# Kernel tuning notes

Hardware: AMD Instinct MI355X
Metric: run time of the kernel (lower is better)

Reference implementation:

```python
import jax, jax.numpy as jnp
import numpy as np

CLASSES = (32, 32)
SUPERCLASSES = 8
OVERALL = CLASSES[0] * CLASSES[1]
CLASS_FACTOR = OVERALL // SUPERCLASSES


def lrelu(x):
    return jax.nn.leaky_relu(x, 0.01)


def conv1x1(x, w, b):
    # x: [B,C,H,W], w: [O,C], b: [O]
    return jnp.einsum('oc,bchw->bohw', w, x) + b[None, :, None, None]


def cond_mul(x, inds, W, b):
    # x: [N,I], inds: [N] int, W: [K,I,O], b: [K,O]
    return jnp.einsum('ni,nio->no', x, W[inds]) + b[inds]


def setup_inputs() -> dict:
    key = jax.random.key(0)
    ks = jax.random.split(key, 24)
    s = 0.05
    d = {}
    d['x_in'] = jax.random.normal(ks[0], (1, 128, 192, 256), dtype=jnp.float32)
    # mask branch
    d['Wm1'] = jax.random.normal(ks[1], (32, 128)) * s
    d['bm1'] = jnp.zeros((32,), jnp.float32)
    d['Wm2'] = jax.random.normal(ks[2], (16, 32)) * s
    d['bm2'] = jnp.zeros((16,), jnp.float32)
    d['Wm3'] = jax.random.normal(ks[3], (1, 16)) * s
    d['bm3'] = jnp.zeros((1,), jnp.float32)
    # classification branch
    d['Wcl1'] = jax.random.normal(ks[4], (128, 128)) * s
    d['bcl1'] = jnp.zeros((128,), jnp.float32)
    d['Wcl21'] = jax.random.normal(ks[5], (128, 128)) * s
    d['bcl21'] = jnp.zeros((128,), jnp.float32)
    d['Wcl31'] = jax.random.normal(ks[6], (32, 128)) * s
    d['bcl31'] = jnp.zeros((32,), jnp.float32)
    d['Wcl22'] = jax.random.normal(ks[7], (CLASSES[0], 128, 32)) * s  # CondMul
    d['bcl22'] = jnp.zeros((CLASSES[0], 32), jnp.float32)
    d['Wcl32'] = jax.random.normal(ks[8], (CLASSES[0], 32, CLASSES[1])) * s
    d['bcl32'] = jnp.zeros((CLASSES[0], CLASSES[1]), jnp.float32)
    d['Wr1'] = jax.random.normal(ks[9], (128, 128)) * s
    d['br1'] = jnp.zeros((128,), jnp.float32)
    d['Wr2'] = jax.random.normal(ks[10], (SUPERCLASSES, 128, 32)) * s
    d['br2'] = jnp.zeros((SUPERCLASSES, 32), jnp.float32)
    d['Wr3'] = jax.random.normal(ks[11], (OVERALL, 32, 1)) * s
    d['br3'] = jnp.zeros((OVERALL, 1), jnp.float32)
    return d


def reference(x_in, Wm1, bm1, Wm2, bm2, Wm3, bm3,
              Wcl1, bcl1, Wcl21, bcl21, Wcl31, bcl31,
              Wcl22, bcl22, Wcl32, bcl32,
              Wr1, br1, Wr2, br2, Wr3, br3):
    B = x_in.shape[0]
    # mask branch
    m = lrelu(conv1x1(x_in, Wm1, bm1))
    m = lrelu(conv1x1(m, Wm2, bm2))
    mask = lrelu(conv1x1(m, Wm3, bm3))
    # classification branch
    x = lrelu(conv1x1(x_in, Wcl1, bcl1))          # [B,128,H,W]
    # torch: transpose(1,3) -> [B,W,H,C], flatten
    x_l = jnp.transpose(x, (0, 3, 2, 1)).reshape(-1, x.shape[1])
    x2 = lrelu(conv1x1(x, Wcl21, bcl21))
    cl1 = conv1x1(x2, Wcl31, bcl31)               # [B,classes0,H,W]
    inds1 = jnp.argmax(cl1, axis=1).reshape(-1).astype(jnp.int32)  # [N] (B,H,W order)
    h = lrelu(cond_mul(x_l, inds1, Wcl22, bcl22))  # [N,32]
    h = cond_mul(h, inds1, Wcl32, bcl32)           # [N,classes1]
    inds2 = jnp.argmax(h, axis=1).astype(jnp.int32)
    inds = inds1 * CLASSES[1] + inds2
    inds_r = jnp.clip(inds, 0, OVERALL - 1).astype(jnp.int32)
    inds_super = jnp.clip(inds_r // CLASS_FACTOR, 0, SUPERCLASSES - 1)
    r = lrelu(conv1x1(x_in, Wr1, br1))
    r_l = jnp.transpose(r, (0, 3, 2, 1)).reshape(-1, r.shape[1])
    r2 = lrelu(cond_mul(r_l, inds_super, Wr2, br2))  # [N,32]
    regression = cond_mul(r2, inds_r, Wr3, br3)      # [N,1]
    regression = regression.reshape(B, 1, 1, -1)
    inds = inds.reshape(regression.shape)
    x_real = (inds.astype(jnp.float32) + regression) * (1.0 / float(OVERALL))
    return (x_real, mask)
```

## Files before the change

kernel.cpp:

```cpp
#include <hip/hip_runtime.h>

#define HH 192
#define WW 256
#define NPIX (HH*WW)
#define NSEG (NPIX/64)

__device__ __forceinline__ float lrelu(float v) { return v > 0.0f ? v : 0.01f * v; }

__device__ __forceinline__ unsigned short bfhi(float x) {
    unsigned b = __float_as_uint(x);
    return (unsigned short)((b + 0x7FFFu + ((b >> 16) & 1u)) >> 16);
}
__device__ __forceinline__ float bff(unsigned short u) {
    return __uint_as_float(((unsigned)u) << 16);
}

typedef __attribute__((ext_vector_type(8))) short short8v;
typedef __attribute__((ext_vector_type(4))) short short4v;
typedef __attribute__((ext_vector_type(4))) float f32x4;

__global__ __launch_bounds__(256, 3) void k_fused1(
    const float* __restrict__ X,
    const float* __restrict__ Wcl1, const float* __restrict__ bcl1,
    const float* __restrict__ Wr1,  const float* __restrict__ br1,
    const float* __restrict__ Wm1,  const float* __restrict__ bm1,
    const float* __restrict__ Wm2,  const float* __restrict__ bm2,
    const float* __restrict__ Wm3,  const float* __restrict__ bm3,
    float* __restrict__ x_t, float* __restrict__ r_t,
    float* __restrict__ out)
{
    __shared__ float smem[10240];

    const int tid = threadIdx.x;
    const int q0  = blockIdx.x * 128;

    if (blockIdx.y == 2) {
        unsigned short* Wmhi = (unsigned short*)smem;
        unsigned short* Wmlo = Wmhi + 1280;
        unsigned short* Xthi = Wmlo + 1280;
        unsigned short* Xtlo = Xthi + 5120;
        float (*m1b)[33] = (float(*)[33])smem;

        const int l = tid & 63;
        const int w = tid >> 6;
        const int c = l & 15;
        const int g = l >> 4;

        float bvm[2][4];
        #pragma unroll
        for (int ot = 0; ot < 2; ++ot)
            #pragma unroll
            for (int r = 0; r < 4; ++r)
                bvm[ot][r] = bm1[ot * 16 + g * 4 + r];

        f32x4 accM[2][2];
        #pragma unroll
        for (int ot = 0; ot < 2; ++ot)
            #pragma unroll
            for (int pi = 0; pi < 2; ++pi) {
                accM[ot][pi][0] = bvm[ot][0]; accM[ot][pi][1] = bvm[ot][1];
                accM[ot][pi][2] = bvm[ot][2]; accM[ot][pi][3] = bvm[ot][3];
            }

        const int sx_px = tid & 127;
        const int sx_kh = (tid >> 7) * 16;
        const float* Xp = X + q0 + sx_px;

        for (int k0 = 0; k0 < 128; k0 += 32) {
            {
                float xv[16];
                #pragma unroll
                for (int i = 0; i < 16; ++i)
                    xv[i] = Xp[(size_t)(k0 + sx_kh + i) * NPIX];
                #pragma unroll
                for (int j = 0; j < 2; ++j) {
                    short8v hv, lv;
                    #pragma unroll
                    for (int i = 0; i < 8; ++i) {
                        unsigned short h = bfhi(xv[j * 8 + i]);
                        hv[i] = (short)h;
                        lv[i] = (short)bfhi(xv[j * 8 + i] - bff(h));
                    }
                    int gg = (sx_kh >> 3) + j;
                    int gs = gg ^ ((sx_px >> 3) & 3);
                    *(short8v*)(Xthi + sx_px * 40 + gs * 8) = hv;
                    *(short8v*)(Xtlo + sx_px * 40 + gs * 8) = lv;
                }
            }
            {
                int o = tid >> 3, kc = (tid & 7) * 4;
                float4 v = *(const float4*)(Wm1 + o * 128 + k0 + kc);
                float wv[4] = {v.x, v.y, v.z, v.w};
                short4v hv, lv;
                #pragma unroll
                for (int i = 0; i < 4; ++i) {
                    unsigned short h = bfhi(wv[i]);
                    hv[i] = (short)h;
                    lv[i] = (short)bfhi(wv[i] - bff(h));
                }
                int gg = kc >> 3;
                int gs = gg ^ (o & 3);
                int addr = o * 40 + gs * 8 + (kc & 7);
                *(short4v*)(Wmhi + addr) = hv;
                *(short4v*)(Wmlo + addr) = lv;
            }
            __syncthreads();

            short8v ahi[2], alo[2];
            #pragma unroll
            for (int ot = 0; ot < 2; ++ot) {
                int row = ot * 16 + c;
                int ao = row * 40 + (g ^ (row & 3)) * 8;
                ahi[ot] = *(const short8v*)(Wmhi + ao);
                alo[ot] = *(const short8v*)(Wmlo + ao);
            }
            #pragma unroll
            for (int pi = 0; pi < 2; ++pi) {
                int row = (2 * w + pi) * 16 + c;
                int bo = row * 40 + (g ^ ((row >> 3) & 3)) * 8;
                short8v bhi = *(const short8v*)(Xthi + bo);
                short8v blo = *(const short8v*)(Xtlo + bo);
                #pragma unroll
                for (int ot = 0; ot < 2; ++ot) {
                    accM[ot][pi] = __builtin_amdgcn_mfma_f32_16x16x32_bf16(
                        ahi[ot], bhi, accM[ot][pi], 0, 0, 0);
                    accM[ot][pi] = __builtin_amdgcn_mfma_f32_16x16x32_bf16(
                        ahi[ot], blo, accM[ot][pi], 0, 0, 0);
                    accM[ot][pi] = __builtin_amdgcn_mfma_f32_16x16x32_bf16(
                        alo[ot], bhi, accM[ot][pi], 0, 0, 0);
                }
            }
            __syncthreads();
        }
        #pragma unroll
        for (int pi = 0; pi < 2; ++pi) {
            int px = (2 * w + pi) * 16 + c;
            #pragma unroll
            for (int ot = 0; ot < 2; ++ot)
                #pragma unroll
                for (int r = 0; r < 4; ++r)
                    m1b[px][ot * 16 + g * 4 + r] = lrelu(accM[ot][pi][r]);
        }
        __syncthreads();
        if (tid < 128) {
            float m3 = bm3[0];
            #pragma unroll 2
            for (int j = 0; j < 16; ++j) {
                float s = bm2[j];
                #pragma unroll
                for (int k = 0; k < 32; ++k)
                    s = fmaf(Wm2[j * 32 + k], m1b[tid][k], s);
                m3 = fmaf(Wm3[j], lrelu(s), m3);
            }
            out[NPIX + q0 + tid] = lrelu(m3);
        }
        return;
    }

    {
        const bool exact = (blockIdx.y == 0);
        const float* __restrict__ Wsrc = exact ? Wcl1 : Wr1;
        const float* __restrict__ bsrc = exact ? bcl1 : br1;
        float* __restrict__ osrc       = exact ? x_t : r_t;

        unsigned short* Whi  = (unsigned short*)smem;
        unsigned short* Wlo  = Whi  + 5120;
        unsigned short* Xthi = Wlo  + 5120;
        unsigned short* Xtlo = Xthi + 5120;

        const int l = tid & 63;
        const int w = tid >> 6;
        const int c = l & 15;
        const int g = l >> 4;
        const int o0 = w * 32;

        float bv[2][4];
        #pragma unroll
        for (int ot = 0; ot < 2; ++ot)
            #pragma unroll
            for (int r = 0; r < 4; ++r)
                bv[ot][r] = bsrc[o0 + ot * 16 + g * 4 + r];

        f32x4 acc[2][8];
        #pragma unroll
        for (int ot = 0; ot < 2; ++ot)
            #pragma unroll
            for (int pt = 0; pt < 8; ++pt) {
                acc[ot][pt][0] = bv[ot][0]; acc[ot][pt][1] = bv[ot][1];
                acc[ot][pt][2] = bv[ot][2]; acc[ot][pt][3] = bv[ot][3];
            }

        const int sx_px = tid & 127;
        const int sx_kh = (tid >> 7) * 16;
        const float* Xp = X + q0 + sx_px;

        for (int k0 = 0; k0 < 128; k0 += 32) {
            {
                float xv[16];
                #pragma unroll
                for (int i = 0; i < 16; ++i)
                    xv[i] = Xp[(size_t)(k0 + sx_kh + i) * NPIX];
                #pragma unroll
                for (int j = 0; j < 2; ++j) {
                    short8v hv, lv;
                    #pragma unroll
                    for (int i = 0; i < 8; ++i) {
                        unsigned short h = bfhi(xv[j * 8 + i]);
                        hv[i] = (short)h;
                        lv[i] = (short)bfhi(xv[j * 8 + i] - bff(h));
                    }
                    int gg = (sx_kh >> 3) + j;
                    int gs = gg ^ ((sx_px >> 3) & 3);
                    *(short8v*)(Xthi + sx_px * 40 + gs * 8) = hv;
                    *(short8v*)(Xtlo + sx_px * 40 + gs * 8) = lv;
                }
            }
            #pragma unroll
            for (int p = 0; p < 4; ++p) {
                int lin = p * 1024 + tid * 4;
                int o = lin >> 5, kc = lin & 31;
                float4 v = *(const float4*)(Wsrc + o * 128 + k0 + kc);
                float wv[4] = {v.x, v.y, v.z, v.w};
                short4v hv, lv;
                #pragma unroll
                for (int i = 0; i < 4; ++i) {
                    unsigned short h = bfhi(wv[i]);
                    hv[i] = (short)h;
                    lv[i] = (short)bfhi(wv[i] - bff(h));
                }
                int gg = kc >> 3;
                int gs = gg ^ (o & 3);
                int addr = o * 40 + gs * 8 + (kc & 7);
                *(short4v*)(Whi + addr) = hv;
                *(short4v*)(Wlo + addr) = lv;
            }
            __syncthreads();

            short8v ahi[2], alo[2];
            #pragma unroll
            for (int ot = 0; ot < 2; ++ot) {
                int row = o0 + ot * 16 + c;
                int ao = row * 40 + (g ^ (row & 3)) * 8;
                ahi[ot] = *(const short8v*)(Whi + ao);
                alo[ot] = *(const short8v*)(Wlo + ao);
            }
            #pragma unroll
            for (int pt = 0; pt < 8; ++pt) {
                int row = pt * 16 + c;
                int bo = row * 40 + (g ^ ((row >> 3) & 3)) * 8;
                short8v bhi = *(const short8v*)(Xthi + bo);
                short8v blo = *(const short8v*)(Xtlo + bo);
                #pragma unroll
                for (int ot = 0; ot < 2; ++ot) {
                    acc[ot][pt] = __builtin_amdgcn_mfma_f32_16x16x32_bf16(
                        ahi[ot], bhi, acc[ot][pt], 0, 0, 0);
                    acc[ot][pt] = __builtin_amdgcn_mfma_f32_16x16x32_bf16(
                        ahi[ot], blo, acc[ot][pt], 0, 0, 0);
                    acc[ot][pt] = __builtin_amdgcn_mfma_f32_16x16x32_bf16(
                        alo[ot], bhi, acc[ot][pt], 0, 0, 0);
                    if (exact)
                        acc[ot][pt] = __builtin_amdgcn_mfma_f32_16x16x32_bf16(
                            alo[ot], blo, acc[ot][pt], 0, 0, 0);
                }
            }
            __syncthreads();
        }

        #pragma unroll
        for (int pt = 0; pt < 8; ++pt) {
            int px = pt * 16 + c;
            int q  = q0 + px;
            int np = (q & 255) * 192 + (q >> 8);
            float* op = osrc + (size_t)np * 128;
            #pragma unroll
            for (int ot = 0; ot < 2; ++ot) {
                float4 o4;
                o4.x = lrelu(acc[ot][pt][0]); o4.y = lrelu(acc[ot][pt][1]);
                o4.z = lrelu(acc[ot][pt][2]); o4.w = lrelu(acc[ot][pt][3]);
                *(float4*)(op + o0 + ot * 16 + g * 4) = o4;
            }
        }
    }
}

__global__ __launch_bounds__(256, 3) void k1b(
    const float* __restrict__ x_t,
    const float* __restrict__ Wcl21, const float* __restrict__ bcl21,
    const float* __restrict__ Wcl31, const float* __restrict__ bcl31,
    int* __restrict__ inds1_q)
{
    __shared__ float smem[8576];
    float (*As)[132]    = (float(*)[132])smem;
    float (*Ws)[132]    = (float(*)[132])(smem + 2112);
    float (*W31)[132]   = (float(*)[132])smem;
    float (*x2t)[68]    = (float(*)[68])(smem + 4224);
    float (*cl1buf)[33] = (float(*)[33])(smem + 4224);

    const int tid = threadIdx.x;
    const int n0  = blockIdx.x * 64;
    const int tcA = tid & 15, trA = tid >> 4;

    float acc[4][8];
    #pragma unroll
    for (int i = 0; i < 4; ++i)
        #pragma unroll
        for (int j = 0; j < 8; ++j)
            acc[i][j] = bcl21[(j >> 2) * 64 + trA * 4 + (j & 3)];

    for (int k0 = 0; k0 < 128; k0 += 16) {
        {
            int lin = tid * 4;
            int px = lin >> 4, kc = lin & 15;
            float4 v = *(const float4*)(x_t + (size_t)(n0 + px) * 128 + k0 + kc);
            As[kc + 0][px] = v.x; As[kc + 1][px] = v.y;
            As[kc + 2][px] = v.z; As[kc + 3][px] = v.w;
        }
        #pragma unroll
        for (int p = 0; p < 2; ++p) {
            int lin = p * 256 + tid;
            int r = lin >> 2, kc = (lin & 3) * 4;
            float4 v = *(const float4*)(Wcl21 + r * 128 + k0 + kc);
            Ws[kc + 0][r] = v.x; Ws[kc + 1][r] = v.y;
            Ws[kc + 2][r] = v.z; Ws[kc + 3][r] = v.w;
        }
        __syncthreads();
        #pragma unroll
        for (int kk = 0; kk < 16; ++kk) {
            float4 a  = *(const float4*)(&As[kk][tcA * 4]);
            float4 w0 = *(const float4*)(&Ws[kk][trA * 4]);
            float4 w1 = *(const float4*)(&Ws[kk][64 + trA * 4]);
            float av[4] = {a.x,a.y,a.z,a.w};
            float wv[8] = {w0.x,w0.y,w0.z,w0.w,w1.x,w1.y,w1.z,w1.w};
            #pragma unroll
            for (int i = 0; i < 4; ++i)
                #pragma unroll
                for (int j = 0; j < 8; ++j)
                    acc[i][j] = fmaf(av[i], wv[j], acc[i][j]);
        }
        __syncthreads();
    }

    const int tcB = tid & 15;
    const int trB = tid >> 4;
    float accB[4][2];
    #pragma unroll
    for (int i = 0; i < 4; ++i)
        #pragma unroll
        for (int j = 0; j < 2; ++j)
            accB[i][j] = bcl31[trB * 2 + j];

    #pragma unroll
    for (int p = 0; p < 4; ++p) {
        int lin = p * 1024 + tid * 4;
        int row = lin >> 7, kc = lin & 127;
        *(float4*)(&W31[row][kc]) = *(const float4*)(Wcl31 + row * 128 + kc);
    }
    #pragma unroll
    for (int j = 0; j < 4; ++j) {
        float4 o;
        o.x = lrelu(acc[0][j]); o.y = lrelu(acc[1][j]);
        o.z = lrelu(acc[2][j]); o.w = lrelu(acc[3][j]);
        *(float4*)(&x2t[trA * 4 + j][tcA * 4]) = o;
    }
    __syncthreads();
    for (int k = 0; k < 64; ++k) {
        float4 a = *(const float4*)(&x2t[k][tcB * 4]);
        float av[4] = {a.x,a.y,a.z,a.w};
        float w0 = W31[trB * 2 + 0][k];
        float w1 = W31[trB * 2 + 1][k];
        #pragma unroll
        for (int i = 0; i < 4; ++i) {
            accB[i][0] = fmaf(av[i], w0, accB[i][0]);
            accB[i][1] = fmaf(av[i], w1, accB[i][1]);
        }
    }
    __syncthreads();
    #pragma unroll
    for (int j = 0; j < 4; ++j) {
        float4 o;
        o.x = lrelu(acc[0][4+j]); o.y = lrelu(acc[1][4+j]);
        o.z = lrelu(acc[2][4+j]); o.w = lrelu(acc[3][4+j]);
        *(float4*)(&x2t[trA * 4 + j][tcA * 4]) = o;
    }
    __syncthreads();
    for (int k = 0; k < 64; ++k) {
        float4 a = *(const float4*)(&x2t[k][tcB * 4]);
        float av[4] = {a.x,a.y,a.z,a.w};
        float w0 = W31[trB * 2 + 0][64 + k];
        float w1 = W31[trB * 2 + 1][64 + k];
        #pragma unroll
        for (int i = 0; i < 4; ++i) {
            accB[i][0] = fmaf(av[i], w0, accB[i][0]);
            accB[i][1] = fmaf(av[i], w1, accB[i][1]);
        }
    }
    __syncthreads();

    #pragma unroll
    for (int i = 0; i < 4; ++i)
        #pragma unroll
        for (int j = 0; j < 2; ++j)
            cl1buf[tcB * 4 + i][trB * 2 + j] = accB[i][j];
    __syncthreads();
    if (tid < 64) {
        float bv = cl1buf[tid][0]; int bi = 0;
        #pragma unroll
        for (int c = 1; c < 32; ++c) {
            float v = cl1buf[tid][c];
            if (v > bv) { bv = v; bi = c; }
        }
        int n = n0 + tid;
        int w = n / 192, hh = n - w * 192;
        inds1_q[hh * 256 + w] = bi;
    }
}

__global__ void k_hist(const int* __restrict__ inds1_q, int* __restrict__ bh) {
    int tid = threadIdx.x;
    int n = blockIdx.x * 256 + tid;
    int key = inds1_q[n];
    int lane = tid & 63;
    int cnt = 0;
    for (int k = 0; k < 32; ++k) {
        unsigned long long m = __ballot(key == k);
        if (lane == k) cnt = __popcll(m);
    }
    if (lane < 32) bh[(n >> 6) * 32 + lane] = cnt;
}

__global__ void k_scanA(const int* __restrict__ bh, int* __restrict__ ebb,
                        int* __restrict__ total) {
    __shared__ int s[256];
    const int k = blockIdx.x, t = threadIdx.x;
    int v0 = bh[(t * 3 + 0) * 32 + k];
    int v1 = bh[(t * 3 + 1) * 32 + k];
    int v2 = bh[(t * 3 + 2) * 32 + k];
    int sum = v0 + v1 + v2;
    s[t] = sum; __syncthreads();
    for (int d = 1; d < 256; d <<= 1) {
        int x = (t >= d) ? s[t - d] : 0;
        __syncthreads();
        s[t] += x;
        __syncthreads();
    }
    int ex = s[t] - sum;
    ebb[(t * 3 + 0) * 32 + k] = ex;
    ebb[(t * 3 + 1) * 32 + k] = ex + v0;
    ebb[(t * 3 + 2) * 32 + k] = ex + v0 + v1;
    if (t == 255) total[k] = s[255];
}

__global__ void k_scatter2(const int* __restrict__ inds1_q,
                           const int* __restrict__ ebb,
                           const int* __restrict__ total,
                           int* __restrict__ order)
{
    __shared__ int ttot[32];
    const int tid = threadIdx.x;
    if (tid < 32) ttot[tid] = total[tid];
    __syncthreads();
    int n = blockIdx.x * 256 + tid;
    int key = inds1_q[n];
    int lane = tid & 63;
    unsigned long long peers = 0;
    for (int k = 0; k < 32; ++k) {
        unsigned long long m = __ballot(key == k);
        if (key == k) peers = m;
    }
    int rank = __popcll(peers & ((1ull << lane) - 1ull));
    int cbase = 0;
    #pragma unroll
    for (int k = 0; k < 32; ++k) cbase += (k < key) ? ttot[k] : 0;
    order[cbase + ebb[(n >> 6) * 32 + key] + rank] = n;
}

__global__ __launch_bounds__(256, 4) void k2h(
    const float* __restrict__ x_t,
    const float* __restrict__ Wcl22, const float* __restrict__ bcl22,
    const float* __restrict__ Wcl32, const float* __restrict__ bcl32,
    const int* __restrict__ total, const int* __restrict__ order,
    int* __restrict__ ind_ord)
{
    __shared__ float Was[4096];
    __shared__ float Wbs[1024];
    __shared__ int cpre[33];
    __shared__ int cbase[33];
    __shared__ int ttot[32];

    const int tid = threadIdx.x;
    if (tid < 32) ttot[tid] = total[tid];
    __syncthreads();
    if (tid == 0) {
        int s = 0, cb = 0;
        for (int k = 0; k < 32; ++k) {
            cpre[k] = s; cbase[k] = cb;
            int c = ttot[k];
            s += (c + 255) >> 8;
            cb += c;
        }
        cpre[32] = s; cbase[32] = cb;
    }
    __syncthreads();
    const int ci = blockIdx.x;
    if (ci >= cpre[32]) return;
    int cls = 0;
    while (cpre[cls + 1] <= ci) ++cls;
    const int st   = (ci - cpre[cls]) * 256;
    const int npx  = min(256, ttot[cls] - st);
    const int base = cbase[cls] + st;

    {
        const float4* ws = (const float4*)(Wcl22 + cls * 4096);
        #pragma unroll
        for (int j = 0; j < 4; ++j) ((float4*)Was)[j * 256 + tid] = ws[j * 256 + tid];
        ((float4*)Wbs)[tid] = ((const float4*)(Wcl32 + cls * 1024))[tid];
    }
    __syncthreads();

    const int m = order[base + min(tid, npx - 1)];
    const float4* xp = (const float4*)(x_t + (size_t)m * 128);

    float h[32];
    #pragma unroll
    for (int j = 0; j < 32; ++j) h[j] = bcl22[cls * 32 + j];
    #pragma unroll 2
    for (int c4 = 0; c4 < 32; ++c4) {
        float4 xv = xp[c4];
        float xa[4] = {xv.x, xv.y, xv.z, xv.w};
        #pragma unroll
        for (int cc = 0; cc < 4; ++cc) {
            const float* wr = &Was[(c4 * 4 + cc) * 32];
            #pragma unroll
            for (int j = 0; j < 32; ++j) h[j] = fmaf(xa[cc], wr[j], h[j]);
        }
    }
    #pragma unroll
    for (int j = 0; j < 32; ++j) h[j] = lrelu(h[j]);

    float g[32];
    #pragma unroll
    for (int j = 0; j < 32; ++j) g[j] = bcl32[cls * 32 + j];
    #pragma unroll 2
    for (int c = 0; c < 32; ++c) {
        float hv = h[c];
        const float* wr = &Wbs[c * 32];
        #pragma unroll
        for (int j = 0; j < 32; ++j) g[j] = fmaf(hv, wr[j], g[j]);
    }
    float bv = g[0]; int bi = 0;
    #pragma unroll
    for (int j = 1; j < 32; ++j)
        if (g[j] > bv) { bv = g[j]; bi = j; }
    if (tid < npx) ind_ord[base + tid] = cls * 32 + bi;
}

__global__ __launch_bounds__(256, 4) void k2r(
    const float* __restrict__ r_t,
    const float* __restrict__ Wr2,  const float* __restrict__ br2,
    const float* __restrict__ Wr3,  const float* __restrict__ br3,
    const int* __restrict__ total, const int* __restrict__ order,
    const int* __restrict__ ind_ord,
    float* __restrict__ out)
{
    __shared__ float Wcs[4096];
    __shared__ int cpre[33];
    __shared__ int cbase[33];
    __shared__ int ttot[32];

    const int tid = threadIdx.x;
    if (tid < 32) ttot[tid] = total[tid];
    __syncthreads();
    if (tid == 0) {
        int s = 0, cb = 0;
        for (int k = 0; k < 32; ++k) {
            cpre[k] = s; cbase[k] = cb;
            int c = ttot[k];
            s += (c + 255) >> 8;
            cb += c;
        }
        cpre[32] = s; cbase[32] = cb;
    }
    __syncthreads();
    const int ci = blockIdx.x;
    if (ci >= cpre[32]) return;
    int cls = 0;
    while (cpre[cls + 1] <= ci) ++cls;
    const int st   = (ci - cpre[cls]) * 256;
    const int npx  = min(256, ttot[cls] - st);
    const int base = cbase[cls] + st;
    const int sup  = cls >> 2;

    {
        const float4* ws = (const float4*)(Wr2 + sup * 4096);
        #pragma unroll
        for (int j = 0; j < 4; ++j) ((float4*)Wcs)[j * 256 + tid] = ws[j * 256 + tid];
    }
    __syncthreads();

    const int li  = min(tid, npx - 1);
    const int m   = order[base + li];
    const int ind = ind_ord[base + li];
    const float4* rp = (const float4*)(r_t + (size_t)m * 128);

    float r2[32];
    #pragma unroll
    for (int j = 0; j < 32; ++j) r2[j] = br2[sup * 32 + j];
    #pragma unroll 2
    for (int c4 = 0; c4 < 32; ++c4) {
        float4 rv = rp[c4];
        float ra[4] = {rv.x, rv.y, rv.z, rv.w};
        #pragma unroll
        for (int cc = 0; cc < 4; ++cc) {
            const float* wr = &Wcs[(c4 * 4 + cc) * 32];
            #pragma unroll
            for (int j = 0; j < 32; ++j) r2[j] = fmaf(ra[cc], wr[j], r2[j]);
        }
    }

    float reg = br3[ind];
    const float* __restrict__ w3 = Wr3 + ind * 32;
    #pragma unroll
    for (int j = 0; j < 32; ++j) reg = fmaf(lrelu(r2[j]), w3[j], reg);

    if (tid < npx) out[m] = ((float)ind + reg) * (1.0f / 1024.0f);
}

extern "C" void kernel_launch(void* const* d_in, const int* in_sizes, int n_in,
                              void* d_out, int out_size, void* d_ws, size_t ws_size,
                              hipStream_t stream)
{
    const float* X     = (const float*)d_in[0];
    const float* Wm1   = (const float*)d_in[1];
    const float* bm1   = (const float*)d_in[2];
    const float* Wm2   = (const float*)d_in[3];
    const float* bm2   = (const float*)d_in[4];
    const float* Wm3   = (const float*)d_in[5];
    const float* bm3   = (const float*)d_in[6];
    const float* Wcl1  = (const float*)d_in[7];
    const float* bcl1  = (const float*)d_in[8];
    const float* Wcl21 = (const float*)d_in[9];
    const float* bcl21 = (const float*)d_in[10];
    const float* Wcl31 = (const float*)d_in[11];
    const float* bcl31 = (const float*)d_in[12];
    const float* Wcl22 = (const float*)d_in[13];
    const float* bcl22 = (const float*)d_in[14];
    const float* Wcl32 = (const float*)d_in[15];
    const float* bcl32 = (const float*)d_in[16];
    const float* Wr1   = (const float*)d_in[17];
    const float* br1   = (const float*)d_in[18];
    const float* Wr2   = (const float*)d_in[19];
    const float* br2   = (const float*)d_in[20];
    const float* Wr3   = (const float*)d_in[21];
    const float* br3   = (const float*)d_in[22];
    float* out = (float*)d_out;

    float* x_t   = (float*)d_ws;
    float* r_t   = x_t + (size_t)NPIX * 128;
    int* inds1_q = (int*)(r_t + (size_t)NPIX * 128);
    int* order   = inds1_q + NPIX;
    int* ind_ord = order + NPIX;
    int* bh      = ind_ord + NPIX;
    int* ebb     = bh + NSEG * 32;
    int* total   = ebb + NSEG * 32;

    k_fused1<<<dim3(NPIX / 128, 3), 256, 0, stream>>>(X, Wcl1, bcl1, Wr1, br1,
                                                      Wm1, bm1, Wm2, bm2, Wm3, bm3,
                                                      x_t, r_t, out);
    k1b<<<NPIX / 64, 256, 0, stream>>>(x_t, Wcl21, bcl21, Wcl31, bcl31, inds1_q);
    k_hist<<<NPIX / 256, 256, 0, stream>>>(inds1_q, bh);
    k_scanA<<<32, 256, 0, stream>>>(bh, ebb, total);
    k_scatter2<<<NPIX / 256, 256, 0, stream>>>(inds1_q, ebb, total, order);
    k2h<<<224, 256, 0, stream>>>(x_t, Wcl22, bcl22, Wcl32, bcl32, total, order, ind_ord);
    k2r<<<224, 256, 0, stream>>>(r_t, Wr2, br2, Wr3, br3, total, order, ind_ord, out);
}
```

Before: 215.2 us.

## Run k1b 128x128 GEMM on bf16 MFMA with hi/lo split for fp32 accuracy

The fp32 FMA GEMM in k1b (x_t times Wcl21) is replaced with bf16 MFMA 16x16x32 instructions. Each operand is split into hi and lo bf16 parts, and four MFMAs per tile approximate fp32 precision. Staging moves to swizzled shared-memory layouts, and the second small GEMM now runs over all 128 channels in one pass instead of two halves. This offloads the main FMA work to the matrix cores. In exchange it uses more shared memory, which may lower occupancy, adds conversion overhead, and slightly changes numerics, which could flip argmax ties.

```diff
diff --git a/kernel.cpp b/kernel.cpp
--- a/kernel.cpp
+++ b/kernel.cpp
@@ -289,81 +289,135 @@
     const float* __restrict__ Wcl31, const float* __restrict__ bcl31,
     int* __restrict__ inds1_q)
 {
-    __shared__ float smem[8576];
-    float (*As)[132]    = (float(*)[132])smem;
-    float (*Ws)[132]    = (float(*)[132])(smem + 2112);
-    float (*W31)[132]   = (float(*)[132])smem;
-    float (*x2t)[68]    = (float(*)[68])(smem + 4224);
-    float (*cl1buf)[33] = (float(*)[33])(smem + 4224);
+    __shared__ float smem[12928];
+    unsigned short* Whi  = (unsigned short*)smem;
+    unsigned short* Wlo  = Whi + 5120;
+    unsigned short* Xthi = Wlo + 5120;
+    unsigned short* Xtlo = Xthi + 2560;
+    float (*x2t)[68]    = (float(*)[68])smem;
+    float (*W31)[132]   = (float(*)[132])(smem + 8704);
+    float (*cl1buf)[33] = (float(*)[33])(smem + 8704);
 
     const int tid = threadIdx.x;
     const int n0  = blockIdx.x * 64;
-    const int tcA = tid & 15, trA = tid >> 4;
-
-    float acc[4][8];
-    #pragma unroll
-    for (int i = 0; i < 4; ++i)
-        #pragma unroll
-        for (int j = 0; j < 8; ++j)
-            acc[i][j] = bcl21[(j >> 2) * 64 + trA * 4 + (j & 3)];
-
-    for (int k0 = 0; k0 < 128; k0 += 16) {
+    const int l = tid & 63, w = tid >> 6;
+    const int c = l & 15, g = l >> 4;
+    const int o0 = w * 32;
+
+    float bv[2][4];
+    #pragma unroll
+    for (int ot = 0; ot < 2; ++ot)
+        #pragma unroll
+        for (int r = 0; r < 4; ++r)
+            bv[ot][r] = bcl21[o0 + ot * 16 + g * 4 + r];
+
+    f32x4 acc[2][4];
+    #pragma unroll
+    for (int ot = 0; ot < 2; ++ot)
+        #pragma unroll
+        for (int pt = 0; pt < 4; ++pt) {
+            acc[ot][pt][0] = bv[ot][0]; acc[ot][pt][1] = bv[ot][1];
+            acc[ot][pt][2] = bv[ot][2]; acc[ot][pt][3] = bv[ot][3];
+        }
+
+    const int sx_px = tid & 63;
+    const int sx_kh = (tid >> 6) * 8;
+    const float* Xp = x_t + (size_t)(n0 + sx_px) * 128 + sx_kh;
+
+    for (int k0 = 0; k0 < 128; k0 += 32) {
         {
-            int lin = tid * 4;
-            int px = lin >> 4, kc = lin & 15;
-            float4 v = *(const float4*)(x_t + (size_t)(n0 + px) * 128 + k0 + kc);
-            As[kc + 0][px] = v.x; As[kc + 1][px] = v.y;
-            As[kc + 2][px] = v.z; As[kc + 3][px] = v.w;
-        }
-        #pragma unroll
-        for (int p = 0; p < 2; ++p) {
-            int lin = p * 256 + tid;
-            int r = lin >> 2, kc = (lin & 3) * 4;
-            float4 v = *(const float4*)(Wcl21 + r * 128 + k0 + kc);
-            Ws[kc + 0][r] = v.x; Ws[kc + 1][r] = v.y;
-            Ws[kc + 2][r] = v.z; Ws[kc + 3][r] = v.w;
+            float4 v0 = *(const float4*)(Xp + k0);
+            float4 v1 = *(const float4*)(Xp + k0 + 4);
+            float xv[8] = {v0.x,v0.y,v0.z,v0.w,v1.x,v1.y,v1.z,v1.w};
+            short8v hv, lv;
+            #pragma unroll
+            for (int i = 0; i < 8; ++i) {
+                unsigned short h = bfhi(xv[i]);
+                hv[i] = (short)h;
+                lv[i] = (short)bfhi(xv[i] - bff(h));
+            }
+            int gg = sx_kh >> 3;
+            int gs = gg ^ ((sx_px >> 3) & 3);
+            *(short8v*)(Xthi + sx_px * 40 + gs * 8) = hv;
+            *(short8v*)(Xtlo + sx_px * 40 + gs * 8) = lv;
+        }
+        #pragma unroll
+        for (int p = 0; p < 4; ++p) {
+            int lin = p * 1024 + tid * 4;
+            int o = lin >> 5, kc = lin & 31;
+            float4 v = *(const float4*)(Wcl21 + o * 128 + k0 + kc);
+            float wv[4] = {v.x, v.y, v.z, v.w};
+            short4v hv, lv;
+            #pragma unroll
+            for (int i = 0; i < 4; ++i) {
+                unsigned short h = bfhi(wv[i]);
+                hv[i] = (short)h;
+                lv[i] = (short)bfhi(wv[i] - bff(h));
+            }
+            int gg = kc >> 3;
+            int gs = gg ^ (o & 3);
+            int addr = o * 40 + gs * 8 + (kc & 7);
+            *(short4v*)(Whi + addr) = hv;
+            *(short4v*)(Wlo + addr) = lv;
         }
         __syncthreads();
-        #pragma unroll
-        for (int kk = 0; kk < 16; ++kk) {
-            float4 a  = *(const float4*)(&As[kk][tcA * 4]);
-            float4 w0 = *(const float4*)(&Ws[kk][trA * 4]);
-            float4 w1 = *(const float4*)(&Ws[kk][64 + trA * 4]);
-            float av[4] = {a.x,a.y,a.z,a.w};
-            float wv[8] = {w0.x,w0.y,w0.z,w0.w,w1.x,w1.y,w1.z,w1.w};
-            #pragma unroll
-            for (int i = 0; i < 4; ++i)
-                #pragma unroll
-                for (int j = 0; j < 8; ++j)
-                    acc[i][j] = fmaf(av[i], wv[j], acc[i][j]);
+
+        short8v ahi[2], alo[2];
+        #pragma unroll
+        for (int ot = 0; ot < 2; ++ot) {
+            int row = o0 + ot * 16 + c;
+            int ao = row * 40 + (g ^ (row & 3)) * 8;
+            ahi[ot] = *(const short8v*)(Whi + ao);
+            alo[ot] = *(const short8v*)(Wlo + ao);
+        }
+        #pragma unroll
+        for (int pt = 0; pt < 4; ++pt) {
+            int row = pt * 16 + c;
+            int bo = row * 40 + (g ^ ((row >> 3) & 3)) * 8;
+            short8v bhi = *(const short8v*)(Xthi + bo);
+            short8v blo = *(const short8v*)(Xtlo + bo);
+            #pragma unroll
+            for (int ot = 0; ot < 2; ++ot) {
+                acc[ot][pt] = __builtin_amdgcn_mfma_f32_16x16x32_bf16(
+                    ahi[ot], bhi, acc[ot][pt], 0, 0, 0);
+                acc[ot][pt] = __builtin_amdgcn_mfma_f32_16x16x32_bf16(
+                    ahi[ot], blo, acc[ot][pt], 0, 0, 0);
+                acc[ot][pt] = __builtin_amdgcn_mfma_f32_16x16x32_bf16(
+                    alo[ot], bhi, acc[ot][pt], 0, 0, 0);
+                acc[ot][pt] = __builtin_amdgcn_mfma_f32_16x16x32_bf16(
+                    alo[ot], blo, acc[ot][pt], 0, 0, 0);
+            }
         }
         __syncthreads();
     }
 
-    const int tcB = tid & 15;
-    const int trB = tid >> 4;
-    float accB[4][2];
-    #pragma unroll
-    for (int i = 0; i < 4; ++i)
-        #pragma unroll
-        for (int j = 0; j < 2; ++j)
-            accB[i][j] = bcl31[trB * 2 + j];
-
+    #pragma unroll
+    for (int pt = 0; pt < 4; ++pt) {
+        int px = pt * 16 + c;
+        #pragma unroll
+        for (int ot = 0; ot < 2; ++ot)
+            #pragma unroll
+            for (int r = 0; r < 4; ++r)
+                x2t[o0 + ot * 16 + g * 4 + r][px] = lrelu(acc[ot][pt][r]);
+    }
     #pragma unroll
     for (int p = 0; p < 4; ++p) {
         int lin = p * 1024 + tid * 4;
         int row = lin >> 7, kc = lin & 127;
         *(float4*)(&W31[row][kc]) = *(const float4*)(Wcl31 + row * 128 + kc);
     }
-    #pragma unroll
-    for (int j = 0; j < 4; ++j) {
-        float4 o;
-        o.x = lrelu(acc[0][j]); o.y = lrelu(acc[1][j]);
-        o.z = lrelu(acc[2][j]); o.w = lrelu(acc[3][j]);
-        *(float4*)(&x2t[trA * 4 + j][tcA * 4]) = o;
-    }
-    __syncthreads();
-    for (int k = 0; k < 64; ++k) {
+    __syncthreads();
+
+    const int tcB = tid & 15;
+    const int trB = tid >> 4;
+    float accB[4][2];
+    #pragma unroll
+    for (int i = 0; i < 4; ++i)
+        #pragma unroll
+        for (int j = 0; j < 2; ++j)
+            accB[i][j] = bcl31[trB * 2 + j];
+
+    for (int k = 0; k < 128; ++k) {
         float4 a = *(const float4*)(&x2t[k][tcB * 4]);
         float av[4] = {a.x,a.y,a.z,a.w};
         float w0 = W31[trB * 2 + 0][k];
@@ -375,26 +429,6 @@
         }
     }
     __syncthreads();
-    #pragma unroll
-    for (int j = 0; j < 4; ++j) {
-        float4 o;
-        o.x = lrelu(acc[0][4+j]); o.y = lrelu(acc[1][4+j]);
-        o.z = lrelu(acc[2][4+j]); o.w = lrelu(acc[3][4+j]);
-        *(float4*)(&x2t[trA * 4 + j][tcA * 4]) = o;
-    }
-    __syncthreads();
-    for (int k = 0; k < 64; ++k) {
-        float4 a = *(const float4*)(&x2t[k][tcB * 4]);
-        float av[4] = {a.x,a.y,a.z,a.w};
-        float w0 = W31[trB * 2 + 0][64 + k];
-        float w1 = W31[trB * 2 + 1][64 + k];
-        #pragma unroll
-        for (int i = 0; i < 4; ++i) {
-            accB[i][0] = fmaf(av[i], w0, accB[i][0]);
-            accB[i][1] = fmaf(av[i], w1, accB[i][1]);
-        }
-    }
-    __syncthreads();
 
     #pragma unroll
     for (int i = 0; i < 4; ++i)
@@ -403,15 +437,15 @@
             cl1buf[tcB * 4 + i][trB * 2 + j] = accB[i][j];
     __syncthreads();
     if (tid < 64) {
-        float bv = cl1buf[tid][0]; int bi = 0;
-        #pragma unroll
-        for (int c = 1; c < 32; ++c) {
-            float v = cl1buf[tid][c];
-            if (v > bv) { bv = v; bi = c; }
+        float bvv = cl1buf[tid][0]; int bi = 0;
+        #pragma unroll
+        for (int cc = 1; cc < 32; ++cc) {
+            float v = cl1buf[tid][cc];
+            if (v > bvv) { bvv = v; bi = cc; }
         }
         int n = n0 + tid;
-        int w = n / 192, hh = n - w * 192;
-        inds1_q[hh * 256 + w] = bi;
+        int ww = n / 192, hh = n - ww * 192;
+        inds1_q[hh * 256 + ww] = bi;
     }
 }
 
```

Result: faster. 199.5 us (median of 2 runs) (-7.3%).
